# Optimization experiments

Measured on AMD Instinct MI355X. Metric: run time of the kernel, lower is better.

The kernel has to match this reference:

```python
import jax, jax.numpy as jnp
import numpy as np

N = 50000       # nodes
E = 1600000     # edges (before self-loops)
DIN = 128       # input_dim
HID = 32        # hidden_dim per head
H = 4           # num_heads
HD = HID * H    # 128, concat-head width
DOUT = 128      # output_dim
NC = 2          # num_classes
G = 256         # graphs in batch
NEG_SLOPE = 0.2
BN_EPS = 1e-5


def setup_inputs() -> dict:
    key = jax.random.key(0)
    ks = jax.random.split(key, 20)
    p = lambda k, shp: (jax.random.normal(k, shp, jnp.float32) * 0.05)
    x = jax.random.normal(ks[0], (N, DIN), jnp.float32)
    edge_index = jax.random.randint(ks[1], (2, E), 0, N, dtype=jnp.int32)
    batch = jnp.sort(jax.random.randint(ks[2], (N,), 0, G, dtype=jnp.int32))
    return {
        "x": x, "edge_index": edge_index, "batch": batch,
        # GATConv 1: lin weight [DIN, H*HID], att vectors [H, HID], bias [H*HID]
        "W1": p(ks[3], (DIN, HD)), "a1_src": p(ks[4], (H, HID)), "a1_dst": p(ks[5], (H, HID)), "b1": p(ks[6], (HD,)),
        "bn1_g": jnp.ones((HD,), jnp.float32), "bn1_b": jnp.zeros((HD,), jnp.float32),
        # GATConv 2: in = H*HID
        "W2": p(ks[7], (HD, HD)), "a2_src": p(ks[8], (H, HID)), "a2_dst": p(ks[9], (H, HID)), "b2": p(ks[10], (HD,)),
        "bn2_g": jnp.ones((HD,), jnp.float32), "bn2_b": jnp.zeros((HD,), jnp.float32),
        "L1W": p(ks[11], (HD, DOUT)), "L1b": p(ks[12], (DOUT,)),
        "L2W": p(ks[13], (DOUT, NC)), "L2b": p(ks[14], (NC,)),
    }


def _add_self_loops(edge_index, n):
    loops = jnp.arange(n, dtype=edge_index.dtype)
    return jnp.concatenate([edge_index, jnp.stack([loops, loops])], axis=1)


def _gat_conv(x, edge_index, W, a_src, a_dst, bias):
    # PyG GATConv: h = x @ W -> [N,H,F]; per-edge score = LeakyReLU(a_src.h_src + a_dst.h_dst);
    # softmax over incoming edges of each dst node; weighted scatter-add; concat heads + bias.
    n = x.shape[0]
    h = (x @ W).reshape(n, H, HID)
    src, dst = edge_index[0], edge_index[1]
    alpha_s = jnp.sum(h * a_src[None], axis=-1)   # [N,H]
    alpha_d = jnp.sum(h * a_dst[None], axis=-1)   # [N,H]
    e = jax.nn.leaky_relu(alpha_s[src] + alpha_d[dst], NEG_SLOPE)  # [E,H]
    m = jax.ops.segment_max(e, dst, num_segments=n)                # stable softmax over neighbors
    ex = jnp.exp(e - m[dst])
    s = jax.ops.segment_sum(ex, dst, num_segments=n)
    alpha = ex / (s[dst] + 1e-16)                                  # [E,H]
    out = jax.ops.segment_sum(h[src] * alpha[:, :, None], dst, num_segments=n)  # [N,H,F]
    return out.reshape(n, H * HID) + bias


def _batch_norm(x, gamma, beta):
    mu = jnp.mean(x, axis=0)
    var = jnp.mean((x - mu) ** 2, axis=0)
    return gamma * (x - mu) * jax.lax.rsqrt(var + BN_EPS) + beta


def reference(x, edge_index, batch, W1, a1_src, a1_dst, b1, bn1_g, bn1_b,
              W2, a2_src, a2_dst, b2, bn2_g, bn2_b, L1W, L1b, L2W, L2b):
    ei = _add_self_loops(edge_index, x.shape[0])
    h = jax.nn.relu(_gat_conv(x, ei, W1, a1_src, a1_dst, b1))
    h = _batch_norm(h, bn1_g, bn1_b)
    h = jax.nn.relu(_gat_conv(h, ei, W2, a2_src, a2_dst, b2))
    h = _batch_norm(h, bn2_g, bn2_b)
    # global mean pool over graph ids
    sums = jax.ops.segment_sum(h, batch, num_segments=G)
    cnts = jax.ops.segment_sum(jnp.ones((h.shape[0],), h.dtype), batch, num_segments=G)
    pooled = sums / jnp.maximum(cnts, 1.0)[:, None]   # [G, HD]
    z = jax.nn.relu(pooled @ L1W + L1b)               # dropout inactive at eval
    return z @ L2W + L2b                              # [G, NC]
```

## Files before the change

### kernel.cpp

```cpp
#include <hip/hip_runtime.h>
#include <math.h>

#define NN 50000
#define EE 1600000
#define GG 256
#define PAD 80
#define NB 256
#define EPB 6250
#define NR 8
#define RNG 6250
#define BCAP 960
#define NSH 16

constexpr float NEG = 0.2f;
constexpr float BN_EPS = 1e-5f;

typedef __attribute__((ext_vector_type(8))) short short8;
typedef __attribute__((ext_vector_type(4))) float f32x4;

constexpr int PB_W1 = 0, PB_A1S = 16384, PB_A1D = 16512, PB_B1 = 16640,
              PB_G1 = 16768, PB_BE1 = 16896, PB_W2 = 17024, PB_A2S = 33408,
              PB_A2D = 33536, PB_B2 = 33664, PB_G2 = 33792, PB_BE2 = 33920,
              PB_L1W = 34048, PB_L1B = 50432, PB_L2W = 50560, PB_L2B = 50816,
              PB_TOTAL = 50818;

struct PtrPack { const void* p[16]; };

__device__ __forceinline__ float b2f(unsigned short u) {
  unsigned v = ((unsigned)u) << 16;
  float f;
  __builtin_memcpy(&f, &v, 4);
  return f;
}
__device__ __forceinline__ float b2f_lo(unsigned u) {
  unsigned v = u << 16;
  float f;
  __builtin_memcpy(&f, &v, 4);
  return f;
}
__device__ __forceinline__ float b2f_hi(unsigned u) {
  unsigned v = u & 0xffff0000u;
  float f;
  __builtin_memcpy(&f, &v, 4);
  return f;
}
__device__ __forceinline__ unsigned short f2b(float f) {
  unsigned x;
  __builtin_memcpy(&x, &f, 4);
  unsigned r = x + 0x7FFFu + ((x >> 16) & 1u);
  return (unsigned short)(r >> 16);
}

__global__ __launch_bounds__(256) void k_prep(PtrPack pk, const unsigned short* __restrict__ xb,
                                              const int* __restrict__ batch,
                                              const int* __restrict__ esrc,
                                              const int* __restrict__ edst,
                                              int* __restrict__ flag,
                                              float* __restrict__ pb,
                                              int* __restrict__ starts, float* __restrict__ bnacc,
                                              int* __restrict__ ctrs,
                                              unsigned char* __restrict__ hist,
                                              unsigned* __restrict__ buck, int* __restrict__ bcnt,
                                              unsigned short* __restrict__ Wt1,
                                              float* __restrict__ wzero,
                                              float* __restrict__ poolsum) {
  const int segoff[17] = {0, 16384, 16512, 16640, 16768, 16896, 17024, 33408,
                          33536, 33664, 33792, 33920, 34048, 50432, 50560, 50816, 50818};
  __shared__ unsigned hcnt[25000];
  __shared__ int bc[NR];
  __shared__ int cs;
  int c = blockIdx.x, t = threadIdx.x;
  if (t == 0) cs = 0;
  if (t < NR) bc[t] = 0;
  for (int j = t; j < 25000; j += 256) hcnt[j] = 0u;
  __syncthreads();
  int sane = 0;
  for (int i = t; i < 4096; i += 256) {
    float a = fabsf(b2f(xb[i]));
    if (a > 1e-4f && a < 100.f) sane++;
  }
  atomicAdd(&cs, sane);
  int e0 = c * EPB;
  for (int i = t; i < EPB; i += 256) {
    int e = e0 + i;
    int d = edst[e];
    if ((unsigned)d >= (unsigned)NN) continue;
    int s = esrc[e];
    if ((unsigned)s >= (unsigned)NN) s = 0;
    int sh = (d & 1) * 16;
    unsigned old = atomicAdd(&hcnt[d >> 1], 1u << sh);
    unsigned rank = (old >> sh) & 0xFFFFu;
    if (rank > 7u) continue;
    int r = d / RNG;
    int dl = d - r * RNG;
    int pos = atomicAdd(&bc[r], 1);
    if (pos < BCAP)
      buck[(c * NR + r) * BCAP + pos] = ((unsigned)s << 16) | ((unsigned)dl << 3) | rank;
  }
  __syncthreads();
  int bf = (cs > 3482) ? 1 : 0;
  if (c == 0 && t == 0) *flag = bf;
  if (t < NR) bcnt[c * NR + t] = min(bc[t], BCAP);
  for (int j = t; j < NN; j += 256) {
    unsigned cc = (hcnt[j >> 1] >> ((j & 1) * 16)) & 0xFFFFu;
    hist[c * NN + j] = (unsigned char)min(cc, 255u);
  }
  for (int j = t; j < 199; j += 256) {
    int i = c * 199 + j;
    if (i < PB_TOTAL) {
      int seg = 0;
      while (i >= segoff[seg + 1]) seg++;
      int k = i - segoff[seg];
      pb[i] = bf ? b2f(((const unsigned short*)pk.p[seg])[k]) : ((const float*)pk.p[seg])[k];
    }
  }
  for (int j = t; j < 64; j += 256) {
    int i = c * 64 + j;
    int n = i & 127, k = i >> 7;
    Wt1[n * 128 + k] = bf ? ((const unsigned short*)pk.p[0])[k * 128 + n]
                          : f2b(((const float*)pk.p[0])[k * 128 + n]);
  }
  for (int j = t; j < 128; j += 256) poolsum[c * 128 + j] = 0.f;
  if (t < 32) bnacc[c * 32 + t] = 0.f;
  for (int j = t; j < 196; j += 256) {
    int n = c * 196 + j;
    if (n < NN) {
      int bb = batch[n];
      bb = min(max(bb, 0), GG - 1);
      int bp = (n == 0) ? -1 : batch[n - 1];
      bp = min(max(bp, -1), GG - 1);
      for (int gg = bp + 1; gg <= bb; gg++) starts[gg] = n;
      if (n == NN - 1)
        for (int gg = bb + 1; gg <= GG; gg++) starts[gg] = NN;
    }
  }
  if (c == 255 && t < 8) ctrs[t] = 0;
}

__global__ __launch_bounds__(256) void k_base(const unsigned char* __restrict__ hist,
                                              unsigned char* __restrict__ base,
                                              int* __restrict__ cnt) {
  int d = blockIdx.x * 256 + threadIdx.x;
  if (d >= NN) return;
  int run = 0;
  for (int b = 0; b < NB; b++) {
    int h = hist[b * NN + d];
    base[b * NN + d] = (unsigned char)min(run, 255);
    run += h;
  }
  cnt[d] = run;
}

__device__ __forceinline__ void gemm_body(float* cst, int bid,
                                          const unsigned short* __restrict__ Xb,
                                          const float* __restrict__ Xf, int bfm,
                                          const unsigned short* __restrict__ Wt,
                                          const float* __restrict__ shiftW,
                                          const float* __restrict__ aS,
                                          const float* __restrict__ aD,
                                          unsigned short* __restrict__ Y,
                                          float* __restrict__ as_, float* __restrict__ ad_) {
  int t = threadIdx.x;
  int row0 = bid * 64;
  int w = t >> 6, lane = t & 63;
  int m = lane & 15, quad = lane >> 4;
  int rA = min(row0 + w * 16 + m, NN - 1);
  short8 a4[4];
  if (bfm) {
    const short8* xp = (const short8*)(Xb + rA * 128);
#pragma unroll
    for (int kk = 0; kk < 4; kk++) a4[kk] = xp[kk * 4 + quad];
  } else {
#pragma unroll
    for (int kk = 0; kk < 4; kk++) {
      const float* xf = Xf + rA * 128 + kk * 32 + quad * 8;
#pragma unroll
      for (int j = 0; j < 8; j++) a4[kk][j] = (short)f2b(xf[j]);
    }
  }
  f32x4 acc[8] = {};
#pragma unroll
  for (int kk = 0; kk < 4; kk++) {
    int ko = kk * 32 + quad * 8;
#pragma unroll
    for (int n0 = 0; n0 < 8; n0++) {
      short8 b = *(const short8*)(Wt + (n0 * 16 + m) * 128 + ko);
      acc[n0] = __builtin_amdgcn_mfma_f32_16x16x32_bf16(a4[kk], b, acc[n0], 0, 0, 0);
    }
  }
#pragma unroll
  for (int n0 = 0; n0 < 8; n0++)
#pragma unroll
    for (int r = 0; r < 4; r++)
      cst[(w * 16 + quad * 4 + r) * 130 + n0 * 16 + m] = acc[n0][r];
  __syncthreads();
  int cg = t & 31, rg = t >> 5;
  int c0 = cg * 4;
  float a_s[4], a_d[4], sw[4];
#pragma unroll
  for (int j = 0; j < 4; j++) {
    a_s[j] = aS[c0 + j];
    a_d[j] = aD[c0 + j];
    sw[j] = shiftW[c0 + j];
  }
#pragma unroll
  for (int i = 0; i < 8; i++) {
    int rl = rg + i * 8;
    int row = row0 + rl;
    float v0 = cst[rl * 130 + c0 + 0] + sw[0];
    float v1 = cst[rl * 130 + c0 + 1] + sw[1];
    float v2 = cst[rl * 130 + c0 + 2] + sw[2];
    float v3 = cst[rl * 130 + c0 + 3] + sw[3];
    if (row < NN) {
      uint2 pk2;
      pk2.x = (unsigned)f2b(v0) | ((unsigned)f2b(v1) << 16);
      pk2.y = (unsigned)f2b(v2) | ((unsigned)f2b(v3) << 16);
      *reinterpret_cast<uint2*>(&Y[row * 128 + c0]) = pk2;
    }
    float ps = v0 * a_s[0] + v1 * a_s[1] + v2 * a_s[2] + v3 * a_s[3];
    float pd = v0 * a_d[0] + v1 * a_d[1] + v2 * a_d[2] + v3 * a_d[3];
    ps += __shfl_xor(ps, 1); ps += __shfl_xor(ps, 2); ps += __shfl_xor(ps, 4);
    pd += __shfl_xor(pd, 1); pd += __shfl_xor(pd, 2); pd += __shfl_xor(pd, 4);
    if ((cg & 7) == 0 && row < NN) {
      int hh = cg >> 3;
      as_[row * 4 + hh] = ps;
      ad_[row * 4 + hh] = pd;
    }
  }
}

__global__ __launch_bounds__(256) void k_fillgemm(const unsigned* __restrict__ buck,
                                                  const int* __restrict__ bcnt,
                                                  const unsigned char* __restrict__ base,
                                                  unsigned short* __restrict__ adj,
                                                  const unsigned short* __restrict__ Xb,
                                                  const float* __restrict__ Xf,
                                                  const int* __restrict__ flagp,
                                                  const unsigned short* __restrict__ Wt,
                                                  const float* __restrict__ shiftW,
                                                  const float* __restrict__ aS,
                                                  const float* __restrict__ aD,
                                                  unsigned short* __restrict__ Y,
                                                  float* __restrict__ as_, float* __restrict__ ad_) {
  __shared__ float cst[64 * 130];
  int idx = blockIdx.x;
  int t = threadIdx.x;
  if (idx < NB) {
    int r = idx & 7, g = idx >> 3;
    int dbase = r * RNG;
#pragma unroll 1
    for (int j = 0; j < 8; j++) {
      int c = g * 8 + j;
      int n = bcnt[c * NR + r];
      const unsigned* bk = buck + (c * NR + r) * BCAP;
      const unsigned char* bs = base + c * NN;
      for (int i = t; i < n; i += 256) {
        unsigned p = bk[i];
        int s = p >> 16;
        int dl = (p >> 3) & 0x1FFF;
        int rank = p & 7;
        int d = dbase + dl;
        int slot = (int)bs[d] + rank;
        if (slot < PAD) adj[d * PAD + slot] = (unsigned short)s;
      }
    }
  } else {
    gemm_body(cst, idx - NB, Xb, Xf, *flagp, Wt, shiftW, aS, aD, Y, as_, ad_);
  }
}

__global__ __launch_bounds__(256) void k_gemm(const unsigned short* __restrict__ Xb,
                                              const unsigned short* __restrict__ Wt,
                                              const float* __restrict__ shiftW,
                                              const float* __restrict__ aS,
                                              const float* __restrict__ aD,
                                              unsigned short* __restrict__ Y,
                                              float* __restrict__ as_, float* __restrict__ ad_) {
  __shared__ float cst[64 * 130];
  gemm_body(cst, blockIdx.x, Xb, nullptr, 1, Wt, shiftW, aS, aD, Y, as_, ad_);
}

__global__ __launch_bounds__(128) void k_agg(const unsigned short* __restrict__ adj,
                                             const int* __restrict__ cnt,
                                             const float4* __restrict__ asrc4,
                                             const float4* __restrict__ adst4,
                                             const uint4* __restrict__ hin4,
                                             const float* __restrict__ bias,
                                             unsigned short* __restrict__ out) {
  int n = blockIdx.x;
  int t = threadIdx.x;
  int deg = cnt[n];
  if (deg < 0) deg = 0;
  if (deg > PAD - 1) deg = PAD - 1;
  int tot = deg + 1;
  int beg = n * PAD;
  __shared__ float w[4][PAD];
  __shared__ int srcs[PAD];
  __shared__ float redv[8][128];
  __shared__ float lsw[2][4];
  float4 ad4 = adst4[n];
  float ls0 = 0.f, ls1 = 0.f, ls2 = 0.f, ls3 = 0.f;
  int g = t >> 4, L = t & 15, hd = L >> 2;
  float acc[8] = {};
  if (t < tot) {
    int s = (t < deg) ? (int)adj[beg + t] : n;
    if ((unsigned)s >= (unsigned)NN) s = n;
    float4 a = asrc4[s];
    float s0 = a.x + ad4.x; s0 = s0 > 0.f ? s0 : NEG * s0;
    float s1 = a.y + ad4.y; s1 = s1 > 0.f ? s1 : NEG * s1;
    float s2 = a.z + ad4.z; s2 = s2 > 0.f ? s2 : NEG * s2;
    float s3 = a.w + ad4.w; s3 = s3 > 0.f ? s3 : NEG * s3;
    ls0 = __expf(s0); ls1 = __expf(s1); ls2 = __expf(s2); ls3 = __expf(s3);
    w[0][t] = ls0; w[1][t] = ls1; w[2][t] = ls2; w[3][t] = ls3;
    srcs[t] = s;
  }
  __syncthreads();
  int e = g;
  for (; e + 24 < tot; e += 32) {
    float w1 = w[hd][e], w2 = w[hd][e + 8], w3 = w[hd][e + 16], w4 = w[hd][e + 24];
    int s1 = srcs[e], s2 = srcs[e + 8], s3 = srcs[e + 16], s4 = srcs[e + 24];
    uint4 v1 = hin4[s1 * 16 + L];
    uint4 v2 = hin4[s2 * 16 + L];
    uint4 v3 = hin4[s3 * 16 + L];
    uint4 v4 = hin4[s4 * 16 + L];
    acc[0] += w1 * b2f_lo(v1.x); acc[1] += w1 * b2f_hi(v1.x);
    acc[2] += w1 * b2f_lo(v1.y); acc[3] += w1 * b2f_hi(v1.y);
    acc[4] += w1 * b2f_lo(v1.z); acc[5] += w1 * b2f_hi(v1.z);
    acc[6] += w1 * b2f_lo(v1.w); acc[7] += w1 * b2f_hi(v1.w);
    acc[0] += w2 * b2f_lo(v2.x); acc[1] += w2 * b2f_hi(v2.x);
    acc[2] += w2 * b2f_lo(v2.y); acc[3] += w2 * b2f_hi(v2.y);
    acc[4] += w2 * b2f_lo(v2.z); acc[5] += w2 * b2f_hi(v2.z);
    acc[6] += w2 * b2f_lo(v2.w); acc[7] += w2 * b2f_hi(v2.w);
    acc[0] += w3 * b2f_lo(v3.x); acc[1] += w3 * b2f_hi(v3.x);
    acc[2] += w3 * b2f_lo(v3.y); acc[3] += w3 * b2f_hi(v3.y);
    acc[4] += w3 * b2f_lo(v3.z); acc[5] += w3 * b2f_hi(v3.z);
    acc[6] += w3 * b2f_lo(v3.w); acc[7] += w3 * b2f_hi(v3.w);
    acc[0] += w4 * b2f_lo(v4.x); acc[1] += w4 * b2f_hi(v4.x);
    acc[2] += w4 * b2f_lo(v4.y); acc[3] += w4 * b2f_hi(v4.y);
    acc[4] += w4 * b2f_lo(v4.z); acc[5] += w4 * b2f_hi(v4.z);
    acc[6] += w4 * b2f_lo(v4.w); acc[7] += w4 * b2f_hi(v4.w);
  }
  for (; e < tot; e += 8) {
    float wv = w[hd][e];
    int s = srcs[e];
    uint4 v = hin4[s * 16 + L];
    acc[0] += wv * b2f_lo(v.x); acc[1] += wv * b2f_hi(v.x);
    acc[2] += wv * b2f_lo(v.y); acc[3] += wv * b2f_hi(v.y);
    acc[4] += wv * b2f_lo(v.z); acc[5] += wv * b2f_hi(v.z);
    acc[6] += wv * b2f_lo(v.w); acc[7] += wv * b2f_hi(v.w);
  }
#pragma unroll
  for (int mm = 1; mm < 64; mm <<= 1) {
    ls0 += __shfl_xor(ls0, mm);
    ls1 += __shfl_xor(ls1, mm);
    ls2 += __shfl_xor(ls2, mm);
    ls3 += __shfl_xor(ls3, mm);
  }
  if ((t & 63) == 0) {
    int wv = t >> 6;
    lsw[wv][0] = ls0; lsw[wv][1] = ls1; lsw[wv][2] = ls2; lsw[wv][3] = ls3;
  }
#pragma unroll
  for (int j = 0; j < 8; j++) redv[g][8 * L + j] = acc[j];
  __syncthreads();
  float den = lsw[0][t >> 5] + lsw[1][t >> 5];
  float sum = 0.f;
#pragma unroll
  for (int g2 = 0; g2 < 8; g2++) sum += redv[g2][t];
  float o = sum / (den + 1e-16f) + bias[t];
  out[n * 128 + t] = f2b(o > 0.f ? o : 0.f);
}

__global__ __launch_bounds__(128) void k_bnstats(const unsigned* __restrict__ x32,
                                                 float* __restrict__ accum, int* __restrict__ ctr,
                                                 const float* __restrict__ g, const float* __restrict__ b,
                                                 float* __restrict__ scale, float* __restrict__ shift,
                                                 const float* __restrict__ W2f, float* __restrict__ sw2,
                                                 unsigned short* __restrict__ Wt2,
                                                 const int* __restrict__ batch,
                                                 float* __restrict__ poolsum) {
  __shared__ int lastflag;
  __shared__ float shs[128];
  __shared__ float scs[128];
  int t = threadIdx.x;
  int c2 = t & 63, half = t >> 6;
  int sh = blockIdx.x & (NSH - 1);
  int r0 = blockIdx.x * 196;
  int r1 = min(r0 + 196, NN);
  float s0 = 0.f, q0 = 0.f, s1 = 0.f, q1 = 0.f;
  if (poolsum) {
    int curg = -1;
    float p0 = 0.f, p1 = 0.f;
    for (int r = r0 + half; r < r1; r += 2) {
      int gg = batch[r];
      gg = min(max(gg, 0), GG - 1);
      if (gg != curg) {
        if (curg >= 0) {
          atomicAdd(&poolsum[curg * 128 + 2 * c2], p0);
          atomicAdd(&poolsum[curg * 128 + 2 * c2 + 1], p1);
        }
        curg = gg; p0 = 0.f; p1 = 0.f;
      }
      unsigned v = x32[r * 64 + c2];
      float lo = b2f_lo(v), hi = b2f_hi(v);
      s0 += lo; q0 += lo * lo; p0 += lo;
      s1 += hi; q1 += hi * hi; p1 += hi;
    }
    if (curg >= 0) {
      atomicAdd(&poolsum[curg * 128 + 2 * c2], p0);
      atomicAdd(&poolsum[curg * 128 + 2 * c2 + 1], p1);
    }
  } else {
    for (int r = r0 + half; r < r1; r += 2) {
      unsigned v = x32[r * 64 + c2];
      float lo = b2f_lo(v), hi = b2f_hi(v);
      s0 += lo; q0 += lo * lo;
      s1 += hi; q1 += hi * hi;
    }
  }
  float* ac = accum + sh * 256;
  atomicAdd(&ac[2 * c2], s0);
  atomicAdd(&ac[2 * c2 + 1], s1);
  atomicAdd(&ac[128 + 2 * c2], q0);
  atomicAdd(&ac[128 + 2 * c2 + 1], q1);
  __threadfence();
  if (t == 0) {
    int done = atomicAdd(ctr, 1);
    lastflag = (done == (int)gridDim.x - 1) ? 1 : 0;
  }
  __syncthreads();
  if (lastflag) {
    float ss = 0.f, qq = 0.f;
#pragma unroll
    for (int s2 = 0; s2 < NSH; s2++) {
      ss += atomicAdd(&accum[s2 * 256 + t], 0.f);
      qq += atomicAdd(&accum[s2 * 256 + 128 + t], 0.f);
    }
    float inv = 1.0f / NN;
    float mu = ss * inv;
    float var = qq * inv - mu * mu;
    float rs = rsqrtf(var + BN_EPS);
    float sc = g[t] * rs;
    float shv = b[t] - mu * sc;
    scale[t] = sc;
    shift[t] = shv;
    shs[t] = shv;
    scs[t] = sc;
    __syncthreads();
    if (W2f) {
      float s = 0.f;
      for (int k = 0; k < 128; k++) s += shs[k] * W2f[k * 128 + t];
      sw2[t] = s;
      for (int i = t; i < 16384; i += 128) {
        int n = i & 127, k = i >> 7;
        Wt2[n * 128 + k] = f2b(scs[k] * W2f[k * 128 + n]);
      }
    }
  }
}

__global__ __launch_bounds__(128) void k_head(const float* __restrict__ poolsum,
                                              const int* __restrict__ starts,
                                              const float* __restrict__ scale, const float* __restrict__ shift,
                                              const float* __restrict__ L1W, const float* __restrict__ L1b,
                                              const float* __restrict__ L2W, const float* __restrict__ L2b,
                                              const int* __restrict__ flagp, void* __restrict__ outp) {
  int g = blockIdx.x, t = threadIdx.x;
  int b0 = starts[g], b1 = starts[g + 1];
  b0 = min(max(b0, 0), NN);
  b1 = min(max(b1, 0), NN);
  int cnt = b1 - b0;
  __shared__ float pooled[128];
  float s = poolsum[g * 128 + t];
  pooled[t] = (cnt > 0) ? (s / cnt) * scale[t] + shift[t] : 0.f;
  __syncthreads();
  float z = L1b[t];
  for (int k = 0; k < 128; k++) z += pooled[k] * L1W[k * 128 + t];
  z = z > 0.f ? z : 0.f;
  __shared__ float r0a[128], r1a[128];
  r0a[t] = z * L2W[t * 2 + 0];
  r1a[t] = z * L2W[t * 2 + 1];
  __syncthreads();
  for (int d = 64; d >= 1; d >>= 1) {
    if (t < d) {
      r0a[t] += r0a[t + d];
      r1a[t] += r1a[t + d];
    }
    __syncthreads();
  }
  if (t == 0) {
    float o0 = r0a[0] + L2b[0];
    float o1 = r1a[0] + L2b[1];
    if (*flagp) {
      unsigned short* ob = (unsigned short*)outp;
      ob[g * 2 + 0] = f2b(o0);
      ob[g * 2 + 1] = f2b(o1);
    } else {
      float* of = (float*)outp;
      of[g * 2 + 0] = o0;
      of[g * 2 + 1] = o1;
    }
  }
}

extern "C" void kernel_launch(void* const* d_in, const int* in_sizes, int n_in,
                              void* d_out, int out_size, void* d_ws, size_t ws_size,
                              hipStream_t stream) {
  (void)in_sizes; (void)n_in; (void)out_size; (void)ws_size;
  const int* ei = (const int*)d_in[1];
  const int* batch = (const int*)d_in[2];

  float* ws = (float*)d_ws;
  size_t o = 0;
  int* flag = (int*)(ws + o);   o += 16;
  int* ctrs = (int*)(ws + o);   o += 16;
  float* pb = ws + o;           o += 51200;
  float* bnacc = ws + o;        o += 8192;
  float* scale1 = ws + o;       o += 128;
  float* shift1 = ws + o;       o += 128;
  float* scale2 = ws + o;       o += 128;
  float* shift2 = ws + o;       o += 128;
  float* wzero = ws + o;        o += 128;
  float* sw2 = ws + o;          o += 128;
  unsigned short* Wt1 = (unsigned short*)(ws + o); o += 8192;
  unsigned short* Wt2 = (unsigned short*)(ws + o); o += 8192;
  float* poolsum = ws + o;      o += GG * 128;
  int* cnt = (int*)(ws + o);    o += 50016;
  int* starts = (int*)(ws + o); o += 512;
  int* bcnt = (int*)(ws + o);   o += 2048;
  float* asrc = ws + o;         o += 200000;
  float* adst = ws + o;         o += 200000;
  unsigned* buck = (unsigned*)(ws + o);            o += NB * NR * BCAP;
  unsigned short* adj = (unsigned short*)(ws + o); o += NN * PAD / 2;
  unsigned short* hA = (unsigned short*)(ws + o);  o += 3200000;
  unsigned short* hB = (unsigned short*)(ws + o);  o += 3200000;

  unsigned char* hist = (unsigned char*)hB;
  unsigned char* base = (unsigned char*)hA;

  const int* esrc = ei;
  const int* edst = ei + EE;

  PtrPack pk;
  for (int i = 0; i < 16; i++) pk.p[i] = d_in[3 + i];

  k_prep<<<NB, 256, 0, stream>>>(pk, (const unsigned short*)d_in[0], batch, esrc, edst,
                                 flag, pb, starts, bnacc, ctrs, hist, buck, bcnt,
                                 Wt1, wzero, poolsum);
  k_base<<<196, 256, 0, stream>>>(hist, base, cnt);

  k_fillgemm<<<NB + 782, 256, 0, stream>>>(buck, bcnt, base, adj,
                                           (const unsigned short*)d_in[0], (const float*)d_in[0],
                                           flag, Wt1, wzero,
                                           pb + PB_A1S, pb + PB_A1D, hB, asrc, adst);
  k_agg<<<NN, 128, 0, stream>>>(adj, cnt, (const float4*)asrc, (const float4*)adst,
                                (const uint4*)hB, pb + PB_B1, hA);
  k_bnstats<<<256, 128, 0, stream>>>((const unsigned*)hA, bnacc, ctrs + 1,
                                     pb + PB_G1, pb + PB_BE1, scale1, shift1,
                                     pb + PB_W2, sw2, Wt2, nullptr, nullptr);

  k_gemm<<<782, 256, 0, stream>>>(hA, Wt2, sw2, pb + PB_A2S, pb + PB_A2D, hB, asrc, adst);
  k_agg<<<NN, 128, 0, stream>>>(adj, cnt, (const float4*)asrc, (const float4*)adst,
                                (const uint4*)hB, pb + PB_B2, hA);
  k_bnstats<<<256, 128, 0, stream>>>((const unsigned*)hA, bnacc + 4096, ctrs + 2,
                                     pb + PB_G2, pb + PB_BE2, scale2, shift2,
                                     nullptr, nullptr, nullptr, batch, poolsum);

  k_head<<<GG, 128, 0, stream>>>(poolsum, starts, scale2, shift2,
                                 pb + PB_L1W, pb + PB_L1B,
                                 pb + PB_L2W, pb + PB_L2B, flag, d_out);
}
```

Baseline: 418.8 us.

## Split GAT aggregation into one block per node-head pair

The aggregation kernel now launches four blocks per node, one per attention head. Each block computes softmax weights for its head only and gathers just that head's 32-channel slice of each neighbour row, with 32 edge groups of 4 lanes. The intent is more parallelism, a lighter per-edge inner loop and better latency hiding. In exchange it launches four times as many blocks, rereads the adjacency list and scores once per head, issues narrower 64-byte gathers per row, and adds an extra reduction stage and sync.

```diff
diff --git a/kernel.cpp b/kernel.cpp
--- a/kernel.cpp
+++ b/kernel.cpp
@@ -280,95 +280,68 @@
   gemm_body(cst, blockIdx.x, Xb, nullptr, 1, Wt, shiftW, aS, aD, Y, as_, ad_);
 }
 
-__global__ __launch_bounds__(128) void k_agg(const unsigned short* __restrict__ adj,
-                                             const int* __restrict__ cnt,
-                                             const float4* __restrict__ asrc4,
-                                             const float4* __restrict__ adst4,
-                                             const uint4* __restrict__ hin4,
-                                             const float* __restrict__ bias,
-                                             unsigned short* __restrict__ out) {
-  int n = blockIdx.x;
+__global__ __launch_bounds__(128) void k_agg4(const unsigned short* __restrict__ adj,
+                                              const int* __restrict__ cnt,
+                                              const float* __restrict__ asrc,
+                                              const float* __restrict__ adst,
+                                              const uint4* __restrict__ hin4,
+                                              const float* __restrict__ bias,
+                                              unsigned short* __restrict__ out) {
+  int bid = blockIdx.x;
+  int pass = bid / NN;
+  int n = bid - pass * NN;
   int t = threadIdx.x;
   int deg = cnt[n];
   if (deg < 0) deg = 0;
   if (deg > PAD - 1) deg = PAD - 1;
   int tot = deg + 1;
-  int beg = n * PAD;
-  __shared__ float w[4][PAD];
-  __shared__ int srcs[PAD];
-  __shared__ float redv[8][128];
-  __shared__ float lsw[2][4];
-  float4 ad4 = adst4[n];
-  float ls0 = 0.f, ls1 = 0.f, ls2 = 0.f, ls3 = 0.f;
-  int g = t >> 4, L = t & 15, hd = L >> 2;
+  __shared__ float w[PAD];
+  __shared__ unsigned short srcs[PAD];
+  __shared__ float redv[32][33];
+  __shared__ float part[4][32];
+  __shared__ float lsw[2];
+  float adh = adst[n * 4 + pass];
+  float lsum = 0.f;
+  if (t < tot) {
+    int s = (t < deg) ? (int)adj[n * PAD + t] : n;
+    if ((unsigned)s >= (unsigned)NN) s = n;
+    float sc = asrc[s * 4 + pass] + adh;
+    sc = sc > 0.f ? sc : NEG * sc;
+    float e = __expf(sc);
+    w[t] = e;
+    srcs[t] = (unsigned short)s;
+    lsum = e;
+  }
+#pragma unroll
+  for (int mm = 1; mm < 64; mm <<= 1) lsum += __shfl_xor(lsum, mm);
+  if ((t & 63) == 0) lsw[t >> 6] = lsum;
+  __syncthreads();
+  float den = lsw[0] + lsw[1];
+  int L = t & 3, g = t >> 2;
   float acc[8] = {};
-  if (t < tot) {
-    int s = (t < deg) ? (int)adj[beg + t] : n;
-    if ((unsigned)s >= (unsigned)NN) s = n;
-    float4 a = asrc4[s];
-    float s0 = a.x + ad4.x; s0 = s0 > 0.f ? s0 : NEG * s0;
-    float s1 = a.y + ad4.y; s1 = s1 > 0.f ? s1 : NEG * s1;
-    float s2 = a.z + ad4.z; s2 = s2 > 0.f ? s2 : NEG * s2;
-    float s3 = a.w + ad4.w; s3 = s3 > 0.f ? s3 : NEG * s3;
-    ls0 = __expf(s0); ls1 = __expf(s1); ls2 = __expf(s2); ls3 = __expf(s3);
-    w[0][t] = ls0; w[1][t] = ls1; w[2][t] = ls2; w[3][t] = ls3;
-    srcs[t] = s;
-  }
-  __syncthreads();
-  int e = g;
-  for (; e + 24 < tot; e += 32) {
-    float w1 = w[hd][e], w2 = w[hd][e + 8], w3 = w[hd][e + 16], w4 = w[hd][e + 24];
-    int s1 = srcs[e], s2 = srcs[e + 8], s3 = srcs[e + 16], s4 = srcs[e + 24];
-    uint4 v1 = hin4[s1 * 16 + L];
-    uint4 v2 = hin4[s2 * 16 + L];
-    uint4 v3 = hin4[s3 * 16 + L];
-    uint4 v4 = hin4[s4 * 16 + L];
-    acc[0] += w1 * b2f_lo(v1.x); acc[1] += w1 * b2f_hi(v1.x);
-    acc[2] += w1 * b2f_lo(v1.y); acc[3] += w1 * b2f_hi(v1.y);
-    acc[4] += w1 * b2f_lo(v1.z); acc[5] += w1 * b2f_hi(v1.z);
-    acc[6] += w1 * b2f_lo(v1.w); acc[7] += w1 * b2f_hi(v1.w);
-    acc[0] += w2 * b2f_lo(v2.x); acc[1] += w2 * b2f_hi(v2.x);
-    acc[2] += w2 * b2f_lo(v2.y); acc[3] += w2 * b2f_hi(v2.y);
-    acc[4] += w2 * b2f_lo(v2.z); acc[5] += w2 * b2f_hi(v2.z);
-    acc[6] += w2 * b2f_lo(v2.w); acc[7] += w2 * b2f_hi(v2.w);
-    acc[0] += w3 * b2f_lo(v3.x); acc[1] += w3 * b2f_hi(v3.x);
-    acc[2] += w3 * b2f_lo(v3.y); acc[3] += w3 * b2f_hi(v3.y);
-    acc[4] += w3 * b2f_lo(v3.z); acc[5] += w3 * b2f_hi(v3.z);
-    acc[6] += w3 * b2f_lo(v3.w); acc[7] += w3 * b2f_hi(v3.w);
-    acc[0] += w4 * b2f_lo(v4.x); acc[1] += w4 * b2f_hi(v4.x);
-    acc[2] += w4 * b2f_lo(v4.y); acc[3] += w4 * b2f_hi(v4.y);
-    acc[4] += w4 * b2f_lo(v4.z); acc[5] += w4 * b2f_hi(v4.z);
-    acc[6] += w4 * b2f_lo(v4.w); acc[7] += w4 * b2f_hi(v4.w);
-  }
-  for (; e < tot; e += 8) {
-    float wv = w[hd][e];
+  for (int e = g; e < tot; e += 32) {
+    float wv = w[e];
     int s = srcs[e];
-    uint4 v = hin4[s * 16 + L];
+    uint4 v = hin4[s * 16 + pass * 4 + L];
     acc[0] += wv * b2f_lo(v.x); acc[1] += wv * b2f_hi(v.x);
     acc[2] += wv * b2f_lo(v.y); acc[3] += wv * b2f_hi(v.y);
     acc[4] += wv * b2f_lo(v.z); acc[5] += wv * b2f_hi(v.z);
     acc[6] += wv * b2f_lo(v.w); acc[7] += wv * b2f_hi(v.w);
   }
 #pragma unroll
-  for (int mm = 1; mm < 64; mm <<= 1) {
-    ls0 += __shfl_xor(ls0, mm);
-    ls1 += __shfl_xor(ls1, mm);
-    ls2 += __shfl_xor(ls2, mm);
-    ls3 += __shfl_xor(ls3, mm);
-  }
-  if ((t & 63) == 0) {
-    int wv = t >> 6;
-    lsw[wv][0] = ls0; lsw[wv][1] = ls1; lsw[wv][2] = ls2; lsw[wv][3] = ls3;
-  }
-#pragma unroll
-  for (int j = 0; j < 8; j++) redv[g][8 * L + j] = acc[j];
-  __syncthreads();
-  float den = lsw[0][t >> 5] + lsw[1][t >> 5];
-  float sum = 0.f;
-#pragma unroll
-  for (int g2 = 0; g2 < 8; g2++) sum += redv[g2][t];
-  float o = sum / (den + 1e-16f) + bias[t];
-  out[n * 128 + t] = f2b(o > 0.f ? o : 0.f);
+  for (int j = 0; j < 8; j++) redv[g][L * 8 + j] = acc[j];
+  __syncthreads();
+  int ch = t & 31, q = t >> 5;
+  float p = 0.f;
+#pragma unroll
+  for (int gg = 0; gg < 8; gg++) p += redv[q * 8 + gg][ch];
+  part[q][ch] = p;
+  __syncthreads();
+  if (t < 32) {
+    float sum = part[0][t] + part[1][t] + part[2][t] + part[3][t];
+    float o = sum / (den + 1e-16f) + bias[pass * 32 + t];
+    out[n * 128 + pass * 32 + t] = f2b(o > 0.f ? o : 0.f);
+  }
 }
 
 __global__ __launch_bounds__(128) void k_bnstats(const unsigned* __restrict__ x32,
@@ -553,15 +526,15 @@
                                            (const unsigned short*)d_in[0], (const float*)d_in[0],
                                            flag, Wt1, wzero,
                                            pb + PB_A1S, pb + PB_A1D, hB, asrc, adst);
-  k_agg<<<NN, 128, 0, stream>>>(adj, cnt, (const float4*)asrc, (const float4*)adst,
-                                (const uint4*)hB, pb + PB_B1, hA);
+  k_agg4<<<4 * NN, 128, 0, stream>>>(adj, cnt, asrc, adst,
+                                     (const uint4*)hB, pb + PB_B1, hA);
   k_bnstats<<<256, 128, 0, stream>>>((const unsigned*)hA, bnacc, ctrs + 1,
                                      pb + PB_G1, pb + PB_BE1, scale1, shift1,
                                      pb + PB_W2, sw2, Wt2, nullptr, nullptr);
 
   k_gemm<<<782, 256, 0, stream>>>(hA, Wt2, sw2, pb + PB_A2S, pb + PB_A2D, hB, asrc, adst);
-  k_agg<<<NN, 128, 0, stream>>>(adj, cnt, (const float4*)asrc, (const float4*)adst,
-                                (const uint4*)hB, pb + PB_B2, hA);
+  k_agg4<<<4 * NN, 128, 0, stream>>>(adj, cnt, asrc, adst,
+                                     (const uint4*)hB, pb + PB_B2, hA);
   k_bnstats<<<256, 128, 0, stream>>>((const unsigned*)hA, bnacc + 4096, ctrs + 2,
                                      pb + PB_G2, pb + PB_BE2, scale2, shift2,
                                      nullptr, nullptr, nullptr, batch, poolsum);
```

Measured after the change: 582.0 us. 1.39x slower.
